# Kernel optimization log

Measured on AMD Instinct MI355X. Metric: run time of the kernel, lower is better.

## Reference

```python
import jax, jax.numpy as jnp
import numpy as np

B, H, W, C = 32, 64, 64, 384
WS = 8            # window size (square)
NH = 12           # num heads
HD = C // NH      # head dim
SCALE = HD ** -0.5


def setup_inputs() -> dict:
    key = jax.random.key(0)
    ks = jax.random.split(key, 5)
    std = 0.02
    return {
        "x": jax.random.normal(ks[0], (B, H, W, C), dtype=jnp.float32),
        "w_qkv": jax.random.normal(ks[1], (C, 3 * C), dtype=jnp.float32) * std,
        "b_qkv": jnp.zeros((3 * C,), dtype=jnp.float32),
        "w_proj": jax.random.normal(ks[2], (C, C), dtype=jnp.float32) * std,
        "b_proj": jnp.zeros((C,), dtype=jnp.float32),
    }


def reference(x, w_qkv, b_qkv, w_proj, b_proj):
    b, h, w, c = x.shape
    nh_win, nw_win = h // WS, w // WS
    # window partition: (B, nh, WS, nw, WS, C) -> (B*nw_total, WS*WS, C)
    xw = x.reshape(b, nh_win, WS, nw_win, WS, c)
    xw = xw.transpose(0, 1, 3, 2, 4, 5).reshape(b * nh_win * nw_win, WS * WS, c)
    nW, T = xw.shape[0], WS * WS
    # qkv projection
    qkv = xw @ w_qkv + b_qkv                      # (nW, T, 3C)
    qkv = qkv.reshape(nW, T, 3, NH, HD).transpose(2, 0, 3, 1, 4)
    q, k, v = qkv[0], qkv[1], qkv[2]              # (nW, NH, T, HD)
    attn = jnp.einsum('wntd,wnsd->wnts', q, k) * SCALE
    attn = jax.nn.softmax(attn, axis=-1)
    out = jnp.einsum('wnts,wnsd->wntd', attn, v)  # (nW, NH, T, HD)
    out = out.transpose(0, 2, 1, 3).reshape(nW, T, c)
    out = out @ w_proj + b_proj
    # window reverse
    out = out.reshape(b, nh_win, nw_win, WS, WS, c)
    out = out.transpose(0, 1, 3, 2, 4, 5).reshape(b, h, w, c)
    return out
```

## Files before the change

### kernel.cpp

```cpp
#include <hip/hip_runtime.h>
#include <hip/hip_bf16.h>

typedef __bf16 bfv8 __attribute__((ext_vector_type(8)));
typedef float f32x4 __attribute__((ext_vector_type(4)));
typedef float fv4 __attribute__((ext_vector_type(4)));
typedef unsigned int u32;

#define MFMA(a,b,c) __builtin_amdgcn_mfma_f32_16x16x32_bf16((a),(b),(c),0,0,0)

constexpr int XW_LD = 392;

__global__ __launch_bounds__(256)
void prep_weights(const float* __restrict__ w_qkv, const float* __restrict__ w_proj,
                  unsigned short* __restrict__ qT, unsigned short* __restrict__ pT)
{
    int i = blockIdx.x * 256 + threadIdx.x;
    const int NQ = 1152 * 384;
    if (i < NQ) {
        int c = i / 384, k = i - c * 384;
        __bf16 h = (__bf16)w_qkv[k * 1152 + c];
        qT[i] = *(unsigned short*)&h;
    } else {
        int j = i - NQ;
        if (j < 384 * 384) {
            int c = j / 384, k = j - c * 384;
            __bf16 h = (__bf16)w_proj[k * 384 + c];
            pT[j] = *(unsigned short*)&h;
        }
    }
}

__device__ __forceinline__ u32 pkbf(float a, float b) {
    __bf16 x = (__bf16)a, y = (__bf16)b;
    unsigned short lo = *(unsigned short*)&x, hi = *(unsigned short*)&y;
    return ((u32)hi << 16) | lo;
}

__device__ __forceinline__ bfv8 conv_frag(u32 p00, u32 p01, u32 p10, u32 p11,
                                          int abase, bool selhi)
{
    union { u32 u[4]; bfv8 v; } cv;
    #pragma unroll
    for (int w = 0; w < 4; ++w) {
        const int addr = abase + (w >> 1) * 64;
        const int lo_ = __builtin_amdgcn_ds_bpermute(addr, (int)((w & 1) ? p01 : p00));
        const int hi_ = __builtin_amdgcn_ds_bpermute(addr, (int)((w & 1) ? p11 : p10));
        cv.u[w] = (u32)(selhi ? hi_ : lo_);
    }
    return cv.v;
}

__global__ __launch_bounds__(256, 3)
void win_attn(const float* __restrict__ x,
              const float* __restrict__ b_qkv,
              const float* __restrict__ b_proj,
              const unsigned short* __restrict__ qT_,
              const unsigned short* __restrict__ pT_,
              float* __restrict__ out)
{
    __shared__ __bf16 sX[64 * XW_LD];

    const __bf16* wqkvT  = (const __bf16*)qT_;
    const __bf16* wprojT = (const __bf16*)pT_;

    const int wid  = blockIdx.x;
    const int bb   = wid >> 6;
    const int wy   = (wid >> 3) & 7;
    const int wx   = wid & 7;
    const int tid  = threadIdx.x;
    const int lane = tid & 63;
    const int wv   = tid >> 6;
    const int lr   = lane & 15;
    const int lg   = lane >> 4;
    const int k8   = lg * 8;

    const size_t gbase = ((size_t)(bb * 64 + wy * 8) * 64 + wx * 8) * 384;

    {
        const float* xb = x + gbase;
        for (int i = tid; i < 64 * 96; i += 256) {
            int t  = i / 96;
            int c4 = (i - t * 96) * 4;
            const fv4 v = __builtin_nontemporal_load(
                (const fv4*)(xb + (size_t)((t >> 3) * 64 + (t & 7)) * 384 + c4));
            *(uint2*)&sX[t * XW_LD + c4] = make_uint2(pkbf(v.x, v.y), pkbf(v.z, v.w));
        }
    }
    __syncthreads();

    const int   abase = ((lg & 1) * 32 + lr) * 4;
    const bool  selhi = (lg & 2) != 0;
    const float SC    = 0.17677669529663687f;

    u32 opk[3][4][2][2];

    #pragma unroll
    for (int hl = 0; hl < 3; ++hl) {
        const int h  = wv * 3 + hl;
        const int cQ = h * 32, cK = cQ + 384, cV = cQ + 768;
        const __bf16* xp = &sX[lr * XW_LD + k8];

        float bQ0[2][4], bK0[2][4], bV0[2];
        #pragma unroll
        for (int hdt = 0; hdt < 2; ++hdt) {
            #pragma unroll
            for (int r = 0; r < 4; ++r) {
                bQ0[hdt][r] = b_qkv[cQ + hdt * 16 + lg * 4 + r];
                bK0[hdt][r] = b_qkv[cK + hdt * 16 + lg * 4 + r];
            }
            bV0[hdt] = b_qkv[cV + hdt * 16 + lr];
        }

        u32 pkQ[2][4][2], pkK[2][4][2], pkV[4][2][2];

        {
            f32x4 acc[2][4];
            #pragma unroll
            for (int a = 0; a < 2; ++a)
                #pragma unroll
                for (int b = 0; b < 4; ++b) acc[a][b] = f32x4{0,0,0,0};
            const __bf16* wp = wqkvT + (size_t)(cQ + lr) * 384 + k8;
            #pragma unroll 6
            for (int kk = 0; kk < 12; ++kk) {
                bfv8 xf[4], wf[2];
                #pragma unroll
                for (int t4 = 0; t4 < 4; ++t4) xf[t4] = *(const bfv8*)(xp + t4 * 16 * XW_LD + kk * 32);
                #pragma unroll
                for (int hdt = 0; hdt < 2; ++hdt) wf[hdt] = *(const bfv8*)(wp + (size_t)hdt * 16 * 384 + kk * 32);
                #pragma unroll
                for (int hdt = 0; hdt < 2; ++hdt)
                    #pragma unroll
                    for (int t4 = 0; t4 < 4; ++t4)
                        acc[hdt][t4] = MFMA(wf[hdt], xf[t4], acc[hdt][t4]);
            }
            #pragma unroll
            for (int hdt = 0; hdt < 2; ++hdt)
                #pragma unroll
                for (int t4 = 0; t4 < 4; ++t4) {
                    pkQ[hdt][t4][0] = pkbf((acc[hdt][t4][0] + bQ0[hdt][0]) * SC, (acc[hdt][t4][1] + bQ0[hdt][1]) * SC);
                    pkQ[hdt][t4][1] = pkbf((acc[hdt][t4][2] + bQ0[hdt][2]) * SC, (acc[hdt][t4][3] + bQ0[hdt][3]) * SC);
                }
        }

        {
            f32x4 acc[2][4];
            #pragma unroll
            for (int a = 0; a < 2; ++a)
                #pragma unroll
                for (int b = 0; b < 4; ++b) acc[a][b] = f32x4{0,0,0,0};
            const __bf16* wp = wqkvT + (size_t)(cK + lr) * 384 + k8;
            #pragma unroll 6
            for (int kk = 0; kk < 12; ++kk) {
                bfv8 xf[4], wf[2];
                #pragma unroll
                for (int t4 = 0; t4 < 4; ++t4) xf[t4] = *(const bfv8*)(xp + t4 * 16 * XW_LD + kk * 32);
                #pragma unroll
                for (int hdt = 0; hdt < 2; ++hdt) wf[hdt] = *(const bfv8*)(wp + (size_t)hdt * 16 * 384 + kk * 32);
                #pragma unroll
                for (int hdt = 0; hdt < 2; ++hdt)
                    #pragma unroll
                    for (int t4 = 0; t4 < 4; ++t4)
                        acc[hdt][t4] = MFMA(wf[hdt], xf[t4], acc[hdt][t4]);
            }
            #pragma unroll
            for (int hdt = 0; hdt < 2; ++hdt)
                #pragma unroll
                for (int t4 = 0; t4 < 4; ++t4) {
                    pkK[hdt][t4][0] = pkbf(acc[hdt][t4][0] + bK0[hdt][0], acc[hdt][t4][1] + bK0[hdt][1]);
                    pkK[hdt][t4][1] = pkbf(acc[hdt][t4][2] + bK0[hdt][2], acc[hdt][t4][3] + bK0[hdt][3]);
                }
        }

        {
            f32x4 acc[4][2];
            #pragma unroll
            for (int a = 0; a < 4; ++a)
                #pragma unroll
                for (int b = 0; b < 2; ++b) acc[a][b] = f32x4{0,0,0,0};
            const __bf16* wp = wqkvT + (size_t)(cV + lr) * 384 + k8;
            #pragma unroll 6
            for (int kk = 0; kk < 12; ++kk) {
                bfv8 xf[4], wf[2];
                #pragma unroll
                for (int t4 = 0; t4 < 4; ++t4) xf[t4] = *(const bfv8*)(xp + t4 * 16 * XW_LD + kk * 32);
                #pragma unroll
                for (int hdt = 0; hdt < 2; ++hdt) wf[hdt] = *(const bfv8*)(wp + (size_t)hdt * 16 * 384 + kk * 32);
                #pragma unroll
                for (int t4 = 0; t4 < 4; ++t4)
                    #pragma unroll
                    for (int hdt = 0; hdt < 2; ++hdt)
                        acc[t4][hdt] = MFMA(xf[t4], wf[hdt], acc[t4][hdt]);
            }
            #pragma unroll
            for (int hdt = 0; hdt < 2; ++hdt) {
                const float bv = bV0[hdt];
                #pragma unroll
                for (int t4 = 0; t4 < 4; ++t4) {
                    pkV[t4][hdt][0] = pkbf(acc[t4][hdt][0] + bv, acc[t4][hdt][1] + bv);
                    pkV[t4][hdt][1] = pkbf(acc[t4][hdt][2] + bv, acc[t4][hdt][3] + bv);
                }
            }
        }

        bfv8 Qf[4];
        #pragma unroll
        for (int qt = 0; qt < 4; ++qt)
            Qf[qt] = conv_frag(pkQ[0][qt][0], pkQ[0][qt][1], pkQ[1][qt][0], pkQ[1][qt][1], abase, selhi);
        f32x4 st[4][4];
        #pragma unroll
        for (int kt = 0; kt < 4; ++kt) {
            const bfv8 kf = conv_frag(pkK[0][kt][0], pkK[0][kt][1], pkK[1][kt][0], pkK[1][kt][1], abase, selhi);
            #pragma unroll
            for (int qt = 0; qt < 4; ++qt) {
                f32x4 z{};
                st[kt][qt] = MFMA(kf, Qf[qt], z);
            }
        }

        float rinv[4];
        #pragma unroll
        for (int qt = 0; qt < 4; ++qt) {
            float mx = -1e30f;
            #pragma unroll
            for (int kt = 0; kt < 4; ++kt)
                #pragma unroll
                for (int r = 0; r < 4; ++r) mx = fmaxf(mx, st[kt][qt][r]);
            mx = fmaxf(mx, __shfl_xor(mx, 16, 64));
            mx = fmaxf(mx, __shfl_xor(mx, 32, 64));
            float sum = 0.f;
            #pragma unroll
            for (int kt = 0; kt < 4; ++kt)
                #pragma unroll
                for (int r = 0; r < 4; ++r) { st[kt][qt][r] = __expf(st[kt][qt][r] - mx); sum += st[kt][qt][r]; }
            sum += __shfl_xor(sum, 16, 64);
            sum += __shfl_xor(sum, 32, 64);
            rinv[qt] = 1.f / sum;
        }
        u32 pkP[4][4][2];
        #pragma unroll
        for (int qt = 0; qt < 4; ++qt)
            #pragma unroll
            for (int kt = 0; kt < 4; ++kt)
                #pragma unroll
                for (int p = 0; p < 2; ++p)
                    pkP[qt][kt][p] = pkbf(st[kt][qt][2 * p] * rinv[qt], st[kt][qt][2 * p + 1] * rinv[qt]);

        bfv8 Vf[2][2];
        #pragma unroll
        for (int ks = 0; ks < 2; ++ks)
            #pragma unroll
            for (int hdt = 0; hdt < 2; ++hdt)
                Vf[ks][hdt] = conv_frag(pkV[2 * ks][hdt][0], pkV[2 * ks][hdt][1],
                                        pkV[2 * ks + 1][hdt][0], pkV[2 * ks + 1][hdt][1], abase, selhi);
        #pragma unroll
        for (int qt = 0; qt < 4; ++qt) {
            bfv8 pf0 = conv_frag(pkP[qt][0][0], pkP[qt][0][1], pkP[qt][1][0], pkP[qt][1][1], abase, selhi);
            bfv8 pf1 = conv_frag(pkP[qt][2][0], pkP[qt][2][1], pkP[qt][3][0], pkP[qt][3][1], abase, selhi);
            f32x4 o0{}, o1{};
            o0 = MFMA(pf0, Vf[0][0], o0);
            o0 = MFMA(pf1, Vf[1][0], o0);
            o1 = MFMA(pf0, Vf[0][1], o1);
            o1 = MFMA(pf1, Vf[1][1], o1);
            opk[hl][qt][0][0] = pkbf(o0[0], o0[1]);
            opk[hl][qt][0][1] = pkbf(o0[2], o0[3]);
            opk[hl][qt][1][0] = pkbf(o1[0], o1[1]);
            opk[hl][qt][1][1] = pkbf(o1[2], o1[3]);
        }
    }

    __syncthreads();

    #pragma unroll
    for (int hl = 0; hl < 3; ++hl)
        #pragma unroll
        for (int qt = 0; qt < 4; ++qt)
            #pragma unroll
            for (int hdt = 0; hdt < 2; ++hdt)
                #pragma unroll
                for (int p = 0; p < 2; ++p) {
                    const u32 u = opk[hl][qt][hdt][p];
                    const int row0 = qt * 16 + lg * 4 + 2 * p;
                    const int col  = (wv * 3 + hl) * 32 + hdt * 16 + lr;
                    unsigned short lo = (unsigned short)(u & 0xffff);
                    unsigned short hi = (unsigned short)(u >> 16);
                    sX[row0 * XW_LD + col]       = *(__bf16*)&lo;
                    sX[(row0 + 1) * XW_LD + col] = *(__bf16*)&hi;
                }
    __syncthreads();

    const int nb = wv * 96;
    float bpj[6];
    #pragma unroll
    for (int nt = 0; nt < 6; ++nt) bpj[nt] = b_proj[nb + nt * 16 + lr];
    f32x4 acc[4][6];
    {
        const __bf16* bp = wprojT + (size_t)(nb + lr) * 384 + k8;
        #pragma unroll
        for (int m = 0; m < 4; ++m)
            #pragma unroll
            for (int nt = 0; nt < 6; ++nt) acc[m][nt] = f32x4{0,0,0,0};
        #pragma unroll 2
        for (int kk = 0; kk < 12; ++kk) {
            bfv8 bfr[6];
            #pragma unroll
            for (int nt = 0; nt < 6; ++nt)
                bfr[nt] = *(const bfv8*)(bp + (size_t)nt * 16 * 384 + kk * 32);
            #pragma unroll
            for (int m = 0; m < 4; ++m) {
                const bfv8 af = *(const bfv8*)&sX[(m * 16 + lr) * XW_LD + kk * 32 + k8];
                #pragma unroll
                for (int nt = 0; nt < 6; ++nt)
                    acc[m][nt] = MFMA(af, bfr[nt], acc[m][nt]);
            }
        }
    }

    __syncthreads();
    float* sF = (float*)sX;
    float* ob = out + gbase;
    #pragma unroll
    for (int half = 0; half < 2; ++half) {
        #pragma unroll
        for (int mm = 0; mm < 2; ++mm) {
            const int m = half * 2 + mm;
            #pragma unroll
            for (int r = 0; r < 4; ++r) {
                const int row = mm * 16 + lg * 4 + r;
                #pragma unroll
                for (int nt = 0; nt < 6; ++nt)
                    sF[row * 384 + nb + nt * 16 + lr] = acc[m][nt][r] + bpj[nt];
            }
        }
        __syncthreads();
        for (int i = tid; i < 32 * 96; i += 256) {
            const int row = i / 96;
            const int c4  = (i - row * 96) * 4;
            const int t   = half * 32 + row;
            const fv4 v = *(const fv4*)&sF[row * 384 + c4];
            __builtin_nontemporal_store(v, (fv4*)(ob + (size_t)((t >> 3) * 64 + (t & 7)) * 384 + c4));
        }
        if (half == 0) __syncthreads();
    }
}

extern "C" void kernel_launch(void* const* d_in, const int* in_sizes, int n_in,
                              void* d_out, int out_size, void* d_ws, size_t ws_size,
                              hipStream_t stream)
{
    const float* x      = (const float*)d_in[0];
    const float* w_qkv  = (const float*)d_in[1];
    const float* b_qkv  = (const float*)d_in[2];
    const float* w_proj = (const float*)d_in[3];
    const float* b_proj = (const float*)d_in[4];
    float* out = (float*)d_out;

    unsigned short* qT = (unsigned short*)d_ws;
    unsigned short* pT = qT + 1152 * 384;

    const int NPREP = 1152 * 384 + 384 * 384;
    prep_weights<<<(NPREP + 255) / 256, 256, 0, stream>>>(w_qkv, w_proj, qT, pT);
    win_attn<<<2048, 256, 0, stream>>>(x, b_qkv, b_proj, qT, pT, out);
}
```

Measured before the change: 385.1 us.

## Split fused window attention into QKV-attention kernel and separate projection GEMM

Splits the single fused kernel into two. The first computes QKV and attention with 6 waves per block (2 heads each, launch bound of 5 blocks) and writes the bf16 attention output to a workspace buffer in image row order. The second runs the output projection as a standalone GEMM reading that buffer from global memory and writing out directly. The goal is higher occupancy and less register pressure than the fused version, at the cost of an extra ~100MB of global memory round trip. The old fused kernel is kept as a fallback when the workspace is too small.

New measurement: 617.3 us. 60.3% more time.

```diff
diff --git a/kernel.cpp b/kernel.cpp
--- a/kernel.cpp
+++ b/kernel.cpp
@@ -5,6 +5,7 @@
 typedef float f32x4 __attribute__((ext_vector_type(4)));
 typedef float fv4 __attribute__((ext_vector_type(4)));
 typedef unsigned int u32;
+typedef unsigned short ush;
 
 #define MFMA(a,b,c) __builtin_amdgcn_mfma_f32_16x16x32_bf16((a),(b),(c),0,0,0)
 
@@ -12,27 +13,27 @@
 
 __global__ __launch_bounds__(256)
 void prep_weights(const float* __restrict__ w_qkv, const float* __restrict__ w_proj,
-                  unsigned short* __restrict__ qT, unsigned short* __restrict__ pT)
+                  ush* __restrict__ qT, ush* __restrict__ pT)
 {
     int i = blockIdx.x * 256 + threadIdx.x;
     const int NQ = 1152 * 384;
     if (i < NQ) {
         int c = i / 384, k = i - c * 384;
         __bf16 h = (__bf16)w_qkv[k * 1152 + c];
-        qT[i] = *(unsigned short*)&h;
+        qT[i] = *(ush*)&h;
     } else {
         int j = i - NQ;
         if (j < 384 * 384) {
             int c = j / 384, k = j - c * 384;
             __bf16 h = (__bf16)w_proj[k * 384 + c];
-            pT[j] = *(unsigned short*)&h;
+            pT[j] = *(ush*)&h;
         }
     }
 }
 
 __device__ __forceinline__ u32 pkbf(float a, float b) {
     __bf16 x = (__bf16)a, y = (__bf16)b;
-    unsigned short lo = *(unsigned short*)&x, hi = *(unsigned short*)&y;
+    ush lo = *(ush*)&x, hi = *(ush*)&y;
     return ((u32)hi << 16) | lo;
 }
 
@@ -50,19 +51,15 @@
     return cv.v;
 }
 
-__global__ __launch_bounds__(256, 3)
-void win_attn(const float* __restrict__ x,
+__global__ __launch_bounds__(384, 5)
+void qkv_attn(const float* __restrict__ x,
               const float* __restrict__ b_qkv,
-              const float* __restrict__ b_proj,
-              const unsigned short* __restrict__ qT_,
-              const unsigned short* __restrict__ pT_,
-              float* __restrict__ out)
+              const ush* __restrict__ qT_,
+              ush* __restrict__ O_)
 {
     __shared__ __bf16 sX[64 * XW_LD];
 
-    const __bf16* wqkvT  = (const __bf16*)qT_;
-    const __bf16* wprojT = (const __bf16*)pT_;
-
+    const __bf16* wqkvT = (const __bf16*)qT_;
     const int wid  = blockIdx.x;
     const int bb   = wid >> 6;
     const int wy   = (wid >> 3) & 7;
@@ -74,32 +71,292 @@
     const int lg   = lane >> 4;
     const int k8   = lg * 8;
 
+    const size_t gbase   = ((size_t)(bb * 64 + wy * 8) * 64 + wx * 8) * 384;
+    const int    rowbase = bb * 4096 + wy * 512 + wx * 8;
+
+    {
+        const float* xb = x + gbase;
+        for (int i = tid; i < 64 * 96; i += 384) {
+            int t  = i / 96;
+            int c4 = (i - t * 96) * 4;
+            const fv4 v = __builtin_nontemporal_load(
+                (const fv4*)(xb + (size_t)((t >> 3) * 64 + (t & 7)) * 384 + c4));
+            *(uint2*)&sX[t * XW_LD + c4] = make_uint2(pkbf(v.x, v.y), pkbf(v.z, v.w));
+        }
+    }
+    __syncthreads();
+
+    const int   abase = ((lg & 1) * 32 + lr) * 4;
+    const bool  selhi = (lg & 2) != 0;
+    const float SC    = 0.17677669529663687f;
+    const __bf16* xp  = &sX[lr * XW_LD + k8];
+
+    #pragma unroll 1
+    for (int hl = 0; hl < 2; ++hl) {
+        const int h  = wv * 2 + hl;
+        const int cQ = h * 32, cK = cQ + 384, cV = cQ + 768;
+
+        u32  pkQ[2][4][2];
+        bfv8 kf[4];
+        bfv8 Vf[2][2];
+
+        {
+            float bQ0[2][4];
+            #pragma unroll
+            for (int hdt = 0; hdt < 2; ++hdt)
+                #pragma unroll
+                for (int r = 0; r < 4; ++r) bQ0[hdt][r] = b_qkv[cQ + hdt * 16 + lg * 4 + r];
+            f32x4 acc[2][4];
+            #pragma unroll
+            for (int a = 0; a < 2; ++a)
+                #pragma unroll
+                for (int b = 0; b < 4; ++b) acc[a][b] = f32x4{0,0,0,0};
+            const __bf16* wp = wqkvT + (size_t)(cQ + lr) * 384 + k8;
+            #pragma unroll 4
+            for (int kk = 0; kk < 12; ++kk) {
+                bfv8 xf[4], wf[2];
+                #pragma unroll
+                for (int t4 = 0; t4 < 4; ++t4) xf[t4] = *(const bfv8*)(xp + t4 * 16 * XW_LD + kk * 32);
+                #pragma unroll
+                for (int hdt = 0; hdt < 2; ++hdt) wf[hdt] = *(const bfv8*)(wp + (size_t)hdt * 16 * 384 + kk * 32);
+                #pragma unroll
+                for (int hdt = 0; hdt < 2; ++hdt)
+                    #pragma unroll
+                    for (int t4 = 0; t4 < 4; ++t4)
+                        acc[hdt][t4] = MFMA(wf[hdt], xf[t4], acc[hdt][t4]);
+            }
+            #pragma unroll
+            for (int hdt = 0; hdt < 2; ++hdt)
+                #pragma unroll
+                for (int t4 = 0; t4 < 4; ++t4) {
+                    pkQ[hdt][t4][0] = pkbf((acc[hdt][t4][0] + bQ0[hdt][0]) * SC, (acc[hdt][t4][1] + bQ0[hdt][1]) * SC);
+                    pkQ[hdt][t4][1] = pkbf((acc[hdt][t4][2] + bQ0[hdt][2]) * SC, (acc[hdt][t4][3] + bQ0[hdt][3]) * SC);
+                }
+        }
+
+        {
+            float bK0[2][4];
+            #pragma unroll
+            for (int hdt = 0; hdt < 2; ++hdt)
+                #pragma unroll
+                for (int r = 0; r < 4; ++r) bK0[hdt][r] = b_qkv[cK + hdt * 16 + lg * 4 + r];
+            f32x4 acc[2][4];
+            #pragma unroll
+            for (int a = 0; a < 2; ++a)
+                #pragma unroll
+                for (int b = 0; b < 4; ++b) acc[a][b] = f32x4{0,0,0,0};
+            const __bf16* wp = wqkvT + (size_t)(cK + lr) * 384 + k8;
+            #pragma unroll 4
+            for (int kk = 0; kk < 12; ++kk) {
+                bfv8 xf[4], wf[2];
+                #pragma unroll
+                for (int t4 = 0; t4 < 4; ++t4) xf[t4] = *(const bfv8*)(xp + t4 * 16 * XW_LD + kk * 32);
+                #pragma unroll
+                for (int hdt = 0; hdt < 2; ++hdt) wf[hdt] = *(const bfv8*)(wp + (size_t)hdt * 16 * 384 + kk * 32);
+                #pragma unroll
+                for (int hdt = 0; hdt < 2; ++hdt)
+                    #pragma unroll
+                    for (int t4 = 0; t4 < 4; ++t4)
+                        acc[hdt][t4] = MFMA(wf[hdt], xf[t4], acc[hdt][t4]);
+            }
+            u32 pkK[2][4][2];
+            #pragma unroll
+            for (int hdt = 0; hdt < 2; ++hdt)
+                #pragma unroll
+                for (int t4 = 0; t4 < 4; ++t4) {
+                    pkK[hdt][t4][0] = pkbf(acc[hdt][t4][0] + bK0[hdt][0], acc[hdt][t4][1] + bK0[hdt][1]);
+                    pkK[hdt][t4][1] = pkbf(acc[hdt][t4][2] + bK0[hdt][2], acc[hdt][t4][3] + bK0[hdt][3]);
+                }
+            #pragma unroll
+            for (int kt = 0; kt < 4; ++kt)
+                kf[kt] = conv_frag(pkK[0][kt][0], pkK[0][kt][1], pkK[1][kt][0], pkK[1][kt][1], abase, selhi);
+        }
+
+        {
+            float bV0[2];
+            #pragma unroll
+            for (int hdt = 0; hdt < 2; ++hdt) bV0[hdt] = b_qkv[cV + hdt * 16 + lr];
+            f32x4 acc[4][2];
+            #pragma unroll
+            for (int a = 0; a < 4; ++a)
+                #pragma unroll
+                for (int b = 0; b < 2; ++b) acc[a][b] = f32x4{0,0,0,0};
+            const __bf16* wp = wqkvT + (size_t)(cV + lr) * 384 + k8;
+            #pragma unroll 4
+            for (int kk = 0; kk < 12; ++kk) {
+                bfv8 xf[4], wf[2];
+                #pragma unroll
+                for (int t4 = 0; t4 < 4; ++t4) xf[t4] = *(const bfv8*)(xp + t4 * 16 * XW_LD + kk * 32);
+                #pragma unroll
+                for (int hdt = 0; hdt < 2; ++hdt) wf[hdt] = *(const bfv8*)(wp + (size_t)hdt * 16 * 384 + kk * 32);
+                #pragma unroll
+                for (int t4 = 0; t4 < 4; ++t4)
+                    #pragma unroll
+                    for (int hdt = 0; hdt < 2; ++hdt)
+                        acc[t4][hdt] = MFMA(xf[t4], wf[hdt], acc[t4][hdt]);
+            }
+            u32 pkV[4][2][2];
+            #pragma unroll
+            for (int hdt = 0; hdt < 2; ++hdt)
+                #pragma unroll
+                for (int t4 = 0; t4 < 4; ++t4) {
+                    pkV[t4][hdt][0] = pkbf(acc[t4][hdt][0] + bV0[hdt], acc[t4][hdt][1] + bV0[hdt]);
+                    pkV[t4][hdt][1] = pkbf(acc[t4][hdt][2] + bV0[hdt], acc[t4][hdt][3] + bV0[hdt]);
+                }
+            #pragma unroll
+            for (int ks = 0; ks < 2; ++ks)
+                #pragma unroll
+                for (int hdt = 0; hdt < 2; ++hdt)
+                    Vf[ks][hdt] = conv_frag(pkV[2 * ks][hdt][0], pkV[2 * ks][hdt][1],
+                                            pkV[2 * ks + 1][hdt][0], pkV[2 * ks + 1][hdt][1], abase, selhi);
+        }
+
+        #pragma unroll
+        for (int qt = 0; qt < 4; ++qt) {
+            const bfv8 Qf = conv_frag(pkQ[0][qt][0], pkQ[0][qt][1], pkQ[1][qt][0], pkQ[1][qt][1], abase, selhi);
+            f32x4 st[4];
+            #pragma unroll
+            for (int kt = 0; kt < 4; ++kt) {
+                f32x4 z{};
+                st[kt] = MFMA(kf[kt], Qf, z);
+            }
+            float mx = -1e30f;
+            #pragma unroll
+            for (int kt = 0; kt < 4; ++kt)
+                #pragma unroll
+                for (int r = 0; r < 4; ++r) mx = fmaxf(mx, st[kt][r]);
+            mx = fmaxf(mx, __shfl_xor(mx, 16, 64));
+            mx = fmaxf(mx, __shfl_xor(mx, 32, 64));
+            float sum = 0.f;
+            #pragma unroll
+            for (int kt = 0; kt < 4; ++kt)
+                #pragma unroll
+                for (int r = 0; r < 4; ++r) { st[kt][r] = __expf(st[kt][r] - mx); sum += st[kt][r]; }
+            sum += __shfl_xor(sum, 16, 64);
+            sum += __shfl_xor(sum, 32, 64);
+            const float rinv = 1.f / sum;
+            u32 pkP[4][2];
+            #pragma unroll
+            for (int kt = 0; kt < 4; ++kt) {
+                pkP[kt][0] = pkbf(st[kt][0] * rinv, st[kt][1] * rinv);
+                pkP[kt][1] = pkbf(st[kt][2] * rinv, st[kt][3] * rinv);
+            }
+            const bfv8 pf0 = conv_frag(pkP[0][0], pkP[0][1], pkP[1][0], pkP[1][1], abase, selhi);
+            const bfv8 pf1 = conv_frag(pkP[2][0], pkP[2][1], pkP[3][0], pkP[3][1], abase, selhi);
+            f32x4 o0{}, o1{};
+            o0 = MFMA(pf0, Vf[0][0], o0);
+            o0 = MFMA(pf1, Vf[1][0], o0);
+            o1 = MFMA(pf0, Vf[0][1], o1);
+            o1 = MFMA(pf1, Vf[1][1], o1);
+            #pragma unroll
+            for (int r = 0; r < 4; ++r) {
+                const int t    = qt * 16 + lg * 4 + r;
+                const int nrow = rowbase + (t >> 3) * 64 + (t & 7);
+                __bf16 a0 = (__bf16)o0[r], a1 = (__bf16)o1[r];
+                O_[(size_t)nrow * 384 + cQ + lr]      = *(ush*)&a0;
+                O_[(size_t)nrow * 384 + cQ + 16 + lr] = *(ush*)&a1;
+            }
+        }
+    }
+}
+
+__global__ __launch_bounds__(256, 3)
+void proj_gemm(const ush* __restrict__ O_,
+               const ush* __restrict__ pT_,
+               const float* __restrict__ b_proj,
+               float* __restrict__ out)
+{
+    const __bf16* Ob = (const __bf16*)O_;
+    const __bf16* wprojT = (const __bf16*)pT_;
+    const int tid  = threadIdx.x;
+    const int lane = tid & 63;
+    const int wv   = tid >> 6;
+    const int lr   = lane & 15;
+    const int lg   = lane >> 4;
+    const int k8   = lg * 8;
+    const int g    = blockIdx.x * 4 + wv;
+    const int row0 = (g >> 2) * 64;
+    const int nb   = (g & 3) * 96;
+
+    const __bf16* ap = Ob + (size_t)(row0 + lr) * 384 + k8;
+    const __bf16* bp = wprojT + (size_t)(nb + lr) * 384 + k8;
+
+    f32x4 acc[4][6];
+    #pragma unroll
+    for (int m = 0; m < 4; ++m)
+        #pragma unroll
+        for (int nt = 0; nt < 6; ++nt) acc[m][nt] = f32x4{0,0,0,0};
+
+    #pragma unroll 3
+    for (int kk = 0; kk < 12; ++kk) {
+        bfv8 bfr[6];
+        #pragma unroll
+        for (int nt = 0; nt < 6; ++nt)
+            bfr[nt] = *(const bfv8*)(bp + (size_t)nt * 16 * 384 + kk * 32);
+        #pragma unroll
+        for (int m = 0; m < 4; ++m) {
+            const bfv8 af = *(const bfv8*)(ap + (size_t)m * 16 * 384 + kk * 32);
+            #pragma unroll
+            for (int nt = 0; nt < 6; ++nt)
+                acc[m][nt] = MFMA(af, bfr[nt], acc[m][nt]);
+        }
+    }
+
+    float bpj[6];
+    #pragma unroll
+    for (int nt = 0; nt < 6; ++nt) bpj[nt] = b_proj[nb + nt * 16 + lr];
+    #pragma unroll
+    for (int m = 0; m < 4; ++m)
+        #pragma unroll
+        for (int r = 0; r < 4; ++r) {
+            float* op = out + (size_t)(row0 + m * 16 + lg * 4 + r) * 384 + nb;
+            #pragma unroll
+            for (int nt = 0; nt < 6; ++nt)
+                op[nt * 16 + lr] = acc[m][nt][r] + bpj[nt];
+        }
+}
+
+__global__ __launch_bounds__(256, 3)
+void win_attn(const float* __restrict__ x,
+              const float* __restrict__ b_qkv,
+              const float* __restrict__ b_proj,
+              const ush* __restrict__ qT_,
+              const ush* __restrict__ pT_,
+              float* __restrict__ out)
+{
+    __shared__ __bf16 sX[64 * XW_LD];
+    const __bf16* wqkvT  = (const __bf16*)qT_;
+    const __bf16* wprojT = (const __bf16*)pT_;
+    const int wid  = blockIdx.x;
+    const int bb   = wid >> 6;
+    const int wy   = (wid >> 3) & 7;
+    const int wx   = wid & 7;
+    const int tid  = threadIdx.x;
+    const int lane = tid & 63;
+    const int wv   = tid >> 6;
+    const int lr   = lane & 15;
+    const int lg   = lane >> 4;
+    const int k8   = lg * 8;
     const size_t gbase = ((size_t)(bb * 64 + wy * 8) * 64 + wx * 8) * 384;
-
     {
         const float* xb = x + gbase;
         for (int i = tid; i < 64 * 96; i += 256) {
             int t  = i / 96;
             int c4 = (i - t * 96) * 4;
-            const fv4 v = __builtin_nontemporal_load(
-                (const fv4*)(xb + (size_t)((t >> 3) * 64 + (t & 7)) * 384 + c4));
+            const fv4 v = *(const fv4*)(xb + (size_t)((t >> 3) * 64 + (t & 7)) * 384 + c4);
             *(uint2*)&sX[t * XW_LD + c4] = make_uint2(pkbf(v.x, v.y), pkbf(v.z, v.w));
         }
     }
     __syncthreads();
-
     const int   abase = ((lg & 1) * 32 + lr) * 4;
     const bool  selhi = (lg & 2) != 0;
     const float SC    = 0.17677669529663687f;
-
     u32 opk[3][4][2][2];
-
     #pragma unroll
     for (int hl = 0; hl < 3; ++hl) {
         const int h  = wv * 3 + hl;
         const int cQ = h * 32, cK = cQ + 384, cV = cQ + 768;
         const __bf16* xp = &sX[lr * XW_LD + k8];
-
         float bQ0[2][4], bK0[2][4], bV0[2];
         #pragma unroll
         for (int hdt = 0; hdt < 2; ++hdt) {
@@ -110,9 +367,7 @@
             }
             bV0[hdt] = b_qkv[cV + hdt * 16 + lr];
         }
-
         u32 pkQ[2][4][2], pkK[2][4][2], pkV[4][2][2];
-
         {
             f32x4 acc[2][4];
             #pragma unroll
@@ -141,7 +396,6 @@
                     pkQ[hdt][t4][1] = pkbf((acc[hdt][t4][2] + bQ0[hdt][2]) * SC, (acc[hdt][t4][3] + bQ0[hdt][3]) * SC);
                 }
         }
-
         {
             f32x4 acc[2][4];
             #pragma unroll
@@ -170,7 +424,6 @@
                     pkK[hdt][t4][1] = pkbf(acc[hdt][t4][2] + bK0[hdt][2], acc[hdt][t4][3] + bK0[hdt][3]);
                 }
         }
-
         {
             f32x4 acc[4][2];
             #pragma unroll
@@ -201,7 +454,6 @@
                 }
             }
         }
-
         bfv8 Qf[4];
         #pragma unroll
         for (int qt = 0; qt < 4; ++qt)
@@ -209,14 +461,13 @@
         f32x4 st[4][4];
         #pragma unroll
         for (int kt = 0; kt < 4; ++kt) {
-            const bfv8 kf = conv_frag(pkK[0][kt][0], pkK[0][kt][1], pkK[1][kt][0], pkK[1][kt][1], abase, selhi);
+            const bfv8 kfr = conv_frag(pkK[0][kt][0], pkK[0][kt][1], pkK[1][kt][0], pkK[1][kt][1], abase, selhi);
             #pragma unroll
             for (int qt = 0; qt < 4; ++qt) {
                 f32x4 z{};
-                st[kt][qt] = MFMA(kf, Qf[qt], z);
-            }
-        }
-
+                st[kt][qt] = MFMA(kfr, Qf[qt], z);
+            }
+        }
         float rinv[4];
         #pragma unroll
         for (int qt = 0; qt < 4; ++qt) {
@@ -244,7 +495,6 @@
                 #pragma unroll
                 for (int p = 0; p < 2; ++p)
                     pkP[qt][kt][p] = pkbf(st[kt][qt][2 * p] * rinv[qt], st[kt][qt][2 * p + 1] * rinv[qt]);
-
         bfv8 Vf[2][2];
         #pragma unroll
         for (int ks = 0; ks < 2; ++ks)
@@ -267,9 +517,7 @@
             opk[hl][qt][1][1] = pkbf(o1[2], o1[3]);
         }
     }
-
     __syncthreads();
-
     #pragma unroll
     for (int hl = 0; hl < 3; ++hl)
         #pragma unroll
@@ -281,13 +529,12 @@
                     const u32 u = opk[hl][qt][hdt][p];
                     const int row0 = qt * 16 + lg * 4 + 2 * p;
                     const int col  = (wv * 3 + hl) * 32 + hdt * 16 + lr;
-                    unsigned short lo = (unsigned short)(u & 0xffff);
-                    unsigned short hi = (unsigned short)(u >> 16);
+                    ush lo = (ush)(u & 0xffff);
+                    ush hi = (ush)(u >> 16);
                     sX[row0 * XW_LD + col]       = *(__bf16*)&lo;
                     sX[(row0 + 1) * XW_LD + col] = *(__bf16*)&hi;
                 }
     __syncthreads();
-
     const int nb = wv * 96;
     float bpj[6];
     #pragma unroll
@@ -314,7 +561,6 @@
             }
         }
     }
-
     __syncthreads();
     float* sF = (float*)sX;
     float* ob = out + gbase;
@@ -354,10 +600,18 @@
     const float* b_proj = (const float*)d_in[4];
     float* out = (float*)d_out;
 
-    unsigned short* qT = (unsigned short*)d_ws;
-    unsigned short* pT = qT + 1152 * 384;
+    ush* qT = (ush*)d_ws;
+    ush* pT = qT + 442368;
+    ush* O  = pT + 147456;
+    const size_t need = (size_t)(442368 + 147456 + 50331648) * 2;
 
     const int NPREP = 1152 * 384 + 384 * 384;
     prep_weights<<<(NPREP + 255) / 256, 256, 0, stream>>>(w_qkv, w_proj, qT, pT);
-    win_attn<<<2048, 256, 0, stream>>>(x, b_qkv, b_proj, qT, pT, out);
+
+    if (ws_size >= need) {
+        qkv_attn<<<2048, 384, 0, stream>>>(x, b_qkv, qT, O);
+        proj_gemm<<<2048, 256, 0, stream>>>(O, pT, b_proj, out);
+    } else {
+        win_attn<<<2048, 256, 0, stream>>>(x, b_qkv, b_proj, qT, pT, out);
+    }
 }
```
